# Performance work log

Measured on AMD Instinct MI355X. Metric: run time of the kernel, lower is better.

Reference implementation:

```python
import jax, jax.numpy as jnp
import numpy as np

N = 100000
E = 3200000


def setup_inputs() -> dict:
    key = jax.random.key(0)
    k1, k2, k3 = jax.random.split(key, 3)
    x = jax.random.normal(k1, (N, 256), dtype=jnp.float32)
    edge_index = jax.random.randint(k2, (2, E), 0, N, dtype=jnp.int64)
    W = jax.random.normal(k3, (256, 64), dtype=jnp.float32) * (1.0 / np.sqrt(256.0))
    b = jnp.zeros((64,), dtype=jnp.float32)
    return {"x": x, "edge_index": edge_index, "W": W, "b": b}


def reference(x, edge_index, W, b):
    # GCNConv (PyG defaults): add self-loops, symmetric deg normalization,
    # linear transform, neighbor aggregation, bias.
    n = x.shape[0]
    loops = jnp.arange(n, dtype=edge_index.dtype)
    row = jnp.concatenate([edge_index[0], loops])  # src
    col = jnp.concatenate([edge_index[1], loops])  # dst

    # degree over destination nodes (incl. self-loops)
    deg = jax.ops.segment_sum(jnp.ones_like(col, dtype=x.dtype), col, num_segments=n)
    deg_inv_sqrt = jnp.where(deg > 0, jax.lax.rsqrt(deg), 0.0)
    norm = deg_inv_sqrt[row] * deg_inv_sqrt[col]  # [E+N]

    h = x @ W  # [N, C]
    msgs = h[row] * norm[:, None]  # gather + scale
    out = jax.ops.segment_sum(msgs, col, num_segments=n)  # scatter-add
    return out + b
```

## Files before the change

kernel.cpp:

```cpp
#include <hip/hip_runtime.h>

#define C_IN 256
#define C_OUT 64
#define BSH 7
#define NPB 128
#define NB 1024
#define CHUNK 4096
#define ROWS 4

typedef short bf16x8 __attribute__((ext_vector_type(8)));
typedef float f32x4 __attribute__((ext_vector_type(4)));

__device__ __forceinline__ unsigned short f2bf(float f) {
    unsigned u = __builtin_bit_cast(unsigned, f);
    u = (u + 0x7FFFu + ((u >> 16) & 1u)) >> 16;
    return (unsigned short)u;
}
__device__ __forceinline__ float bflo(unsigned u) {
    return __builtin_bit_cast(float, u << 16);
}
__device__ __forceinline__ float bfhi(unsigned u) {
    return __builtin_bit_cast(float, u & 0xffff0000u);
}

__global__ __launch_bounds__(256) void k_wt(const float* __restrict__ W,
                                            unsigned short* __restrict__ WTs) {
#pragma unroll
    for (int i = 0; i < 16; ++i) {
        int f = i * 256 + threadIdx.x;
        int k = f >> 4;
        int n4 = (f & 15) * 4;
        float4 v = ((const float4*)W)[f];
        int c = k >> 3, ci = k & 7;
        float vv[4] = {v.x, v.y, v.z, v.w};
#pragma unroll
        for (int r = 0; r < 4; ++r) {
            int row = n4 + r;
            WTs[row * 256 + ((c ^ (row & 7)) << 3) + ci] = f2bf(vv[r]);
        }
    }
}

__global__ __launch_bounds__(1024) void k_hist2(const int* __restrict__ dst,
                                                int* __restrict__ table, int e) {
    __shared__ int cnt[NB];
    if (threadIdx.x < NB) cnt[threadIdx.x] = 0;
    __syncthreads();
    int b0 = blockIdx.x * CHUNK;
#pragma unroll
    for (int k = 0; k < CHUNK / 1024; ++k) {
        int i = b0 + k * 1024 + threadIdx.x;
        if (i < e) atomicAdd(&cnt[dst[i] >> BSH], 1);
    }
    __syncthreads();
    if (threadIdx.x < NB) table[(size_t)blockIdx.x * NB + threadIdx.x] = cnt[threadIdx.x];
}

__global__ __launch_bounds__(256) void kA2(int* __restrict__ table,
                                           int* __restrict__ tot, int nbin) {
    __shared__ int part[256];
    int bucket = blockIdx.x;
    int t = threadIdx.x;
    int v[ROWS];
    int s = 0;
#pragma unroll
    for (int i = 0; i < ROWS; ++i) {
        int r = t * ROWS + i;
        int x = (r < nbin) ? table[(size_t)r * NB + bucket] : 0;
        v[i] = s;
        s += x;
    }
    part[t] = s;
    __syncthreads();
    for (int off = 1; off < 256; off <<= 1) {
        int u = (t >= off) ? part[t - off] : 0;
        __syncthreads();
        part[t] += u;
        __syncthreads();
    }
    int base = part[t] - s;
#pragma unroll
    for (int i = 0; i < ROWS; ++i) {
        int r = t * ROWS + i;
        if (r < nbin) table[(size_t)r * NB + bucket] = v[i] + base;
    }
    if (t == 255) tot[bucket] = part[255];
}

__global__ __launch_bounds__(1024) void kB(const int* __restrict__ tot,
                                           int* __restrict__ gbase, int e) {
    __shared__ int l[NB];
    int t = threadIdx.x;
    int v = tot[t];
    l[t] = v;
    __syncthreads();
    for (int off = 1; off < NB; off <<= 1) {
        int u = (t >= off) ? l[t - off] : 0;
        __syncthreads();
        l[t] += u;
        __syncthreads();
    }
    gbase[t] = l[t] - v;
    if (t == NB - 1) gbase[NB] = e;
}

__global__ __launch_bounds__(1024) void k_bin2(const int* __restrict__ src,
                                               const int* __restrict__ dst,
                                               const int* __restrict__ table,
                                               const int* __restrict__ gbase,
                                               int* __restrict__ sorted, int e) {
    __shared__ int cur[NB];
    if (threadIdx.x < NB)
        cur[threadIdx.x] = table[(size_t)blockIdx.x * NB + threadIdx.x] + gbase[threadIdx.x];
    __syncthreads();
    int b0 = blockIdx.x * CHUNK;
#pragma unroll
    for (int k = 0; k < CHUNK / 1024; ++k) {
        int i = b0 + k * 1024 + threadIdx.x;
        if (i < e) {
            int d = dst[i];
            int bb = d >> BSH;
            int off = atomicAdd(&cur[bb], 1);
            sorted[off] = (src[i] << BSH) | (d & (NPB - 1));
        }
    }
}

__global__ __launch_bounds__(512) void k_sort2(const int* __restrict__ sorted,
                                               const int* __restrict__ gbase,
                                               int* __restrict__ eidx,
                                               int* __restrict__ rowptr,
                                               float* __restrict__ dinv, int n, int e) {
    __shared__ int cnt[NPB];
    __shared__ int sc[NPB];
    __shared__ int cur[NPB];
    int b = blockIdx.x;
    int node0 = b * NPB;
    int range = min(NPB, n - node0);
    int inbase = gbase[b];
    int m_b = gbase[b + 1] - inbase;
    if (threadIdx.x < NPB) cnt[threadIdx.x] = 0;
    __syncthreads();
    for (int j = threadIdx.x; j < m_b; j += 512)
        atomicAdd(&cnt[sorted[inbase + j] & (NPB - 1)], 1);
    __syncthreads();
    if (threadIdx.x < NPB) sc[threadIdx.x] = cnt[threadIdx.x];
    __syncthreads();
    for (int off = 1; off < NPB; off <<= 1) {
        int t = (threadIdx.x < NPB && threadIdx.x >= off) ? sc[threadIdx.x - off] : 0;
        __syncthreads();
        if (threadIdx.x < NPB) sc[threadIdx.x] += t;
        __syncthreads();
    }
    if (threadIdx.x < NPB) {
        int excl = inbase + sc[threadIdx.x] - cnt[threadIdx.x];
        cur[threadIdx.x] = excl;
        if (threadIdx.x < range) {
            rowptr[node0 + threadIdx.x] = excl;
            dinv[node0 + threadIdx.x] = rsqrtf((float)(cnt[threadIdx.x] + 1));
        }
    }
    __syncthreads();
    for (int j = threadIdx.x; j < m_b; j += 512) {
        int v = sorted[inbase + j];
        int pos = atomicAdd(&cur[v & (NPB - 1)], 1);
        eidx[pos] = v >> BSH;
    }
    if (b == 0 && threadIdx.x == 0) rowptr[n] = e;
}

__global__ __launch_bounds__(256, 3) void k_gemm(const float* __restrict__ x,
                                                 const unsigned short* __restrict__ WTs,
                                                 const float* __restrict__ dinv,
                                                 unsigned short* __restrict__ h, int n) {
    __shared__ unsigned short Wl[64 * 256];

    const int t = threadIdx.x;
    const int lane = t & 63;
    const int wv = t >> 6;
    const int m = lane & 15;
    const int q = lane >> 4;
    const int mx = m & 7;

#pragma unroll
    for (int j = 0; j < 8; ++j) {
        const unsigned short* gsrc = WTs + j * 2048 + wv * 512 + lane * 8;
        unsigned short* ldst = Wl + j * 2048 + wv * 512;
        __builtin_amdgcn_global_load_lds(
            (const __attribute__((address_space(1))) unsigned int*)gsrc,
            (__attribute__((address_space(3))) unsigned int*)ldst, 16, 0, 0);
    }

    int arow = blockIdx.x * 64 + 16 * wv + m;
    const float* xp = x + (size_t)(arow < n ? arow : 0) * C_IN + q * 8;
    float4 raw[16];
#pragma unroll
    for (int ks = 0; ks < 8; ++ks) {
        const float* p0 = xp + ks * 32;
        const float* p1 = xp + ks * 32 + 4;
        asm volatile("global_load_dwordx4 %0, %1, off" : "=v"(raw[2 * ks]) : "v"(p0));
        asm volatile("global_load_dwordx4 %0, %1, off" : "=v"(raw[2 * ks + 1]) : "v"(p1));
    }

    asm volatile("s_waitcnt vmcnt(0)" ::: "memory");
    __builtin_amdgcn_sched_barrier(0);
    __syncthreads();

    float di[4];
#pragma unroll
    for (int r = 0; r < 4; ++r) {
        int gr = blockIdx.x * 64 + 16 * wv + q * 4 + r;
        di[r] = dinv[gr < n ? gr : 0];
    }

    bf16x8 A[8];
#pragma unroll
    for (int ks = 0; ks < 8; ++ks) {
        float4 v0 = raw[2 * ks];
        float4 v1 = raw[2 * ks + 1];
        bf16x8 a;
        a[0] = (short)f2bf(v0.x); a[1] = (short)f2bf(v0.y);
        a[2] = (short)f2bf(v0.z); a[3] = (short)f2bf(v0.w);
        a[4] = (short)f2bf(v1.x); a[5] = (short)f2bf(v1.y);
        a[6] = (short)f2bf(v1.z); a[7] = (short)f2bf(v1.w);
        A[ks] = a;
    }

    f32x4 acc[4];
#pragma unroll
    for (int nt = 0; nt < 4; ++nt) acc[nt] = (f32x4){0.f, 0.f, 0.f, 0.f};

#pragma unroll
    for (int ks = 0; ks < 8; ++ks) {
        int c = ks * 4 + q;
        int cs = (c ^ mx) << 3;
#pragma unroll
        for (int nt = 0; nt < 4; ++nt) {
            bf16x8 B = *(const bf16x8*)&Wl[(nt * 16 + m) * 256 + cs];
            acc[nt] = __builtin_amdgcn_mfma_f32_16x16x32_bf16(A[ks], B, acc[nt], 0, 0, 0);
        }
    }

#pragma unroll
    for (int r = 0; r < 4; ++r) {
        int gr = blockIdx.x * 64 + 16 * wv + q * 4 + r;
        if (gr < n) {
#pragma unroll
            for (int nt = 0; nt < 4; ++nt)
                h[(size_t)gr * C_OUT + nt * 16 + m] = f2bf(acc[nt][r] * di[r]);
        }
    }
}

__global__ __launch_bounds__(256) void k_gather(const int* __restrict__ rowptr,
                                                const int* __restrict__ eidx,
                                                const unsigned short* __restrict__ h,
                                                const float* __restrict__ dinv,
                                                const float* __restrict__ bias,
                                                float* __restrict__ out, int n) {
    int node = blockIdx.x * 4 + (threadIdx.x >> 6);
    if (node >= n) return;
    int lane = threadIdx.x & 63;
    int g = lane >> 3;
    int c8 = (lane & 7) * 8;

    int beg = rowptr[node];
    int end = rowptr[node + 1];
    float a0 = 0.f, a1 = 0.f, a2 = 0.f, a3 = 0.f;
    float a4 = 0.f, a5 = 0.f, a6 = 0.f, a7 = 0.f;

    int j = beg;
    for (; j + 15 < end; j += 16) {
        int sa = eidx[j + g];
        int sb = eidx[j + 8 + g];
        uint4 ha = *(const uint4*)&h[(size_t)sa * C_OUT + c8];
        uint4 hb = *(const uint4*)&h[(size_t)sb * C_OUT + c8];
        a0 += bflo(ha.x); a1 += bfhi(ha.x); a2 += bflo(ha.y); a3 += bfhi(ha.y);
        a4 += bflo(ha.z); a5 += bfhi(ha.z); a6 += bflo(ha.w); a7 += bfhi(ha.w);
        a0 += bflo(hb.x); a1 += bfhi(hb.x); a2 += bflo(hb.y); a3 += bfhi(hb.y);
        a4 += bflo(hb.z); a5 += bfhi(hb.z); a6 += bflo(hb.w); a7 += bfhi(hb.w);
    }
    for (; j < end; j += 8) {
        int rem = end - j;
        int idx = j + ((g < rem) ? g : 0);
        int s = eidx[idx];
        float mq = (g < rem) ? 1.f : 0.f;
        uint4 hv = *(const uint4*)&h[(size_t)s * C_OUT + c8];
        a0 += bflo(hv.x) * mq; a1 += bfhi(hv.x) * mq;
        a2 += bflo(hv.y) * mq; a3 += bfhi(hv.y) * mq;
        a4 += bflo(hv.z) * mq; a5 += bfhi(hv.z) * mq;
        a6 += bflo(hv.w) * mq; a7 += bfhi(hv.w) * mq;
    }
#pragma unroll
    for (int off = 8; off < 64; off <<= 1) {
        a0 += __shfl_xor(a0, off, 64); a1 += __shfl_xor(a1, off, 64);
        a2 += __shfl_xor(a2, off, 64); a3 += __shfl_xor(a3, off, 64);
        a4 += __shfl_xor(a4, off, 64); a5 += __shfl_xor(a5, off, 64);
        a6 += __shfl_xor(a6, off, 64); a7 += __shfl_xor(a7, off, 64);
    }
    if (g == 0) {
        float di = dinv[node];
        uint4 sv = *(const uint4*)&h[(size_t)node * C_OUT + c8];
        float4 b0 = *(const float4*)&bias[c8];
        float4 b1 = *(const float4*)&bias[c8 + 4];
        float4 o0, o1;
        o0.x = (a0 + bflo(sv.x)) * di + b0.x;
        o0.y = (a1 + bfhi(sv.x)) * di + b0.y;
        o0.z = (a2 + bflo(sv.y)) * di + b0.z;
        o0.w = (a3 + bfhi(sv.y)) * di + b0.w;
        o1.x = (a4 + bflo(sv.z)) * di + b1.x;
        o1.y = (a5 + bfhi(sv.z)) * di + b1.y;
        o1.z = (a6 + bflo(sv.w)) * di + b1.z;
        o1.w = (a7 + bfhi(sv.w)) * di + b1.w;
        *(float4*)&out[(size_t)node * C_OUT + c8] = o0;
        *(float4*)&out[(size_t)node * C_OUT + c8 + 4] = o1;
    }
}

extern "C" void kernel_launch(void* const* d_in, const int* in_sizes, int n_in,
                              void* d_out, int out_size, void* d_ws, size_t ws_size,
                              hipStream_t stream) {
    const float* x = (const float*)d_in[0];
    const int* ei = (const int*)d_in[1];
    const float* W = (const float*)d_in[2];
    const float* bias = (const float*)d_in[3];
    float* out = (float*)d_out;

    const int n = in_sizes[0] / C_IN;
    const int e = in_sizes[1] / 2;
    const int* src = ei;
    const int* dst = ei + e;

    const int nbin = (e + CHUNK - 1) / CHUNK;
    const int nbuck = (n + NPB - 1) / NPB;

    char* w = (char*)d_ws;
    unsigned short* h = (unsigned short*)w;  w += (size_t)n * C_OUT * 2;
    int* sorted = (int*)w;                   w += (size_t)e * 4;
    int* eidx = (int*)w;                     w += (size_t)e * 4;
    float* dinv = (float*)w;                 w += (size_t)n * 4;
    int* rowptr = (int*)w;                   w += (size_t)(n + 1) * 4;
    int* table = (int*)w;                    w += (size_t)nbin * NB * 4;
    int* tot = (int*)w;                      w += NB * 4;
    int* gbase = (int*)w;                    w += (NB + 1) * 4;
    unsigned short* WTs = (unsigned short*)w; w += (size_t)C_OUT * C_IN * 2;

    k_wt<<<1, 256, 0, stream>>>(W, WTs);
    k_hist2<<<nbin, 1024, 0, stream>>>(dst, table, e);
    kA2<<<NB, 256, 0, stream>>>(table, tot, nbin);
    kB<<<1, 1024, 0, stream>>>(tot, gbase, e);
    k_bin2<<<nbin, 1024, 0, stream>>>(src, dst, table, gbase, sorted, e);
    k_sort2<<<nbuck, 512, 0, stream>>>(sorted, gbase, eidx, rowptr, dinv, n, e);
    k_gemm<<<(n + 63) / 64, 256, 0, stream>>>(x, WTs, dinv, h, n);
    k_gather<<<(n + 3) / 4, 256, 0, stream>>>(rowptr, eidx, h, dinv, bias, out, n);
}
```

Baseline: 337.5 us.

## Batch neighbor index loads per wave and issue up to eight gathers before waiting

The gather kernel now loads up to 64 edge indices per wave in one coalesced read, broadcasts them with shuffles, and issues up to eight 16-byte row loads before a single wait. This raises memory-level parallelism for the random row gathers. Masking is replaced by a zeroed sentinel row at index n that is written by the GEMM kernel, so the workspace grows by one row. Nodes with at most 32 edges skip the second group of four loads. The inline asm plus the manual vmcnt wait keep more registers live and depend on the sentinel being written before the gather kernel runs.

```diff
diff --git a/kernel.cpp b/kernel.cpp
--- a/kernel.cpp
+++ b/kernel.cpp
@@ -182,6 +182,9 @@
     const int q = lane >> 4;
     const int mx = m & 7;
 
+    if (blockIdx.x == 0 && t < 8)
+        *(uint4*)&h[(size_t)n * C_OUT + t * 8] = make_uint4(0u, 0u, 0u, 0u);
+
 #pragma unroll
     for (int j = 0; j < 8; ++j) {
         const unsigned short* gsrc = WTs + j * 2048 + wv * 512 + lane * 8;
@@ -251,6 +254,18 @@
         }
     }
 }
+
+#define GROUND(T, HV)                                                                   \
+    {                                                                                   \
+        int s_ = __shfl(eid, (T) * 8 + g, 64);                                          \
+        const unsigned short* p_ = h + (size_t)s_ * C_OUT + c8;                         \
+        asm volatile("global_load_dwordx4 %0, %1, off" : "=v"(HV) : "v"(p_));           \
+    }
+#define ACC8(HV)                                                                        \
+    {                                                                                   \
+        a0 += bflo(HV.x); a1 += bfhi(HV.x); a2 += bflo(HV.y); a3 += bfhi(HV.y);         \
+        a4 += bflo(HV.z); a5 += bfhi(HV.z); a6 += bflo(HV.w); a7 += bfhi(HV.w);         \
+    }
 
 __global__ __launch_bounds__(256) void k_gather(const int* __restrict__ rowptr,
                                                 const int* __restrict__ eidx,
@@ -266,31 +281,36 @@
 
     int beg = rowptr[node];
     int end = rowptr[node + 1];
+    int cnt = end - beg;
+
     float a0 = 0.f, a1 = 0.f, a2 = 0.f, a3 = 0.f;
     float a4 = 0.f, a5 = 0.f, a6 = 0.f, a7 = 0.f;
 
-    int j = beg;
-    for (; j + 15 < end; j += 16) {
-        int sa = eidx[j + g];
-        int sb = eidx[j + 8 + g];
-        uint4 ha = *(const uint4*)&h[(size_t)sa * C_OUT + c8];
-        uint4 hb = *(const uint4*)&h[(size_t)sb * C_OUT + c8];
-        a0 += bflo(ha.x); a1 += bfhi(ha.x); a2 += bflo(ha.y); a3 += bfhi(ha.y);
-        a4 += bflo(ha.z); a5 += bfhi(ha.z); a6 += bflo(ha.w); a7 += bfhi(ha.w);
-        a0 += bflo(hb.x); a1 += bfhi(hb.x); a2 += bflo(hb.y); a3 += bfhi(hb.y);
-        a4 += bflo(hb.z); a5 += bfhi(hb.z); a6 += bflo(hb.w); a7 += bfhi(hb.w);
-    }
-    for (; j < end; j += 8) {
-        int rem = end - j;
-        int idx = j + ((g < rem) ? g : 0);
-        int s = eidx[idx];
-        float mq = (g < rem) ? 1.f : 0.f;
-        uint4 hv = *(const uint4*)&h[(size_t)s * C_OUT + c8];
-        a0 += bflo(hv.x) * mq; a1 += bfhi(hv.x) * mq;
-        a2 += bflo(hv.y) * mq; a3 += bfhi(hv.y) * mq;
-        a4 += bflo(hv.z) * mq; a5 += bfhi(hv.z) * mq;
-        a6 += bflo(hv.w) * mq; a7 += bfhi(hv.w) * mq;
-    }
+    {
+        int idx = beg + lane;
+        int eid = (idx < end) ? eidx[idx] : n;
+        uint4 hv0, hv1, hv2, hv3, hv4, hv5, hv6, hv7;
+        GROUND(0, hv0); GROUND(1, hv1); GROUND(2, hv2); GROUND(3, hv3);
+        bool more = cnt > 32;
+        if (more) { GROUND(4, hv4); GROUND(5, hv5); GROUND(6, hv6); GROUND(7, hv7); }
+        asm volatile("s_waitcnt vmcnt(0)" ::: "memory");
+        __builtin_amdgcn_sched_barrier(0);
+        ACC8(hv0); ACC8(hv1); ACC8(hv2); ACC8(hv3);
+        if (more) { ACC8(hv4); ACC8(hv5); ACC8(hv6); ACC8(hv7); }
+    }
+    for (int j = beg + 64; j < end; j += 64) {
+        int idx = j + lane;
+        int eid = (idx < end) ? eidx[idx] : n;
+        uint4 hv0, hv1, hv2, hv3, hv4, hv5, hv6, hv7;
+        GROUND(0, hv0); GROUND(1, hv1); GROUND(2, hv2); GROUND(3, hv3);
+        bool more = (end - j) > 32;
+        if (more) { GROUND(4, hv4); GROUND(5, hv5); GROUND(6, hv6); GROUND(7, hv7); }
+        asm volatile("s_waitcnt vmcnt(0)" ::: "memory");
+        __builtin_amdgcn_sched_barrier(0);
+        ACC8(hv0); ACC8(hv1); ACC8(hv2); ACC8(hv3);
+        if (more) { ACC8(hv4); ACC8(hv5); ACC8(hv6); ACC8(hv7); }
+    }
+
 #pragma unroll
     for (int off = 8; off < 64; off <<= 1) {
         a0 += __shfl_xor(a0, off, 64); a1 += __shfl_xor(a1, off, 64);
@@ -335,7 +355,7 @@
     const int nbuck = (n + NPB - 1) / NPB;
 
     char* w = (char*)d_ws;
-    unsigned short* h = (unsigned short*)w;  w += (size_t)n * C_OUT * 2;
+    unsigned short* h = (unsigned short*)w;  w += ((size_t)n + 1) * C_OUT * 2;
     int* sorted = (int*)w;                   w += (size_t)e * 4;
     int* eidx = (int*)w;                     w += (size_t)e * 4;
     float* dinv = (float*)w;                 w += (size_t)n * 4;
```

Result: faster. 329.0 us (-2.5%).
